# Kernel tuning notes

Measured on AMD Instinct MI355X. Metric: run time of the kernel, lower is better.

## Reference

```python
import jax, jax.numpy as jnp
import numpy as np

B, L, D = 64, 2048, 1024
P, C = 512, 32  # proj_dim = D // 2, score_dim = output_dim
INIT_SCALE = 0.05  # keras 'uniform' init: U(-0.05, 0.05)


def _uniform(key, shape):
    return jax.random.uniform(key, shape, jnp.float32, -INIT_SCALE, INIT_SCALE)


def setup_inputs() -> dict:
    key = jax.random.key(0)
    ks = jax.random.split(key, 8)
    encoded_sentence = jax.random.normal(ks[0], (B, L, D), jnp.float32)
    # indices in [1, L-2] so prep-1 and prep+1 are in bounds
    prep_indices = jax.random.randint(ks[1], (B, 1), 1, L - 1, jnp.int32)
    return {
        "encoded_sentence": encoded_sentence,
        "prep_indices": prep_indices,
        "proj_head": _uniform(ks[2], (D, P)),
        "proj_prep": _uniform(ks[3], (D, P)),
        "proj_child": _uniform(ks[4], (D, P)),
        "hidden_w": _uniform(ks[5], (P, P)),
        "scorer": _uniform(ks[6], (P, C)),
    }


def reference(encoded_sentence, prep_indices, proj_head, proj_prep, proj_child, hidden_w, scorer):
    # encoded_sentence: [B, L, D]; prep_indices: [B, 1]
    prep = prep_indices[:, 0]                      # [B]
    b = jnp.arange(encoded_sentence.shape[0])      # [B]
    head_enc = encoded_sentence[b, prep - 1, :]    # [B, D] (head = token before prep)
    prep_enc = encoded_sentence[b, prep, :]        # [B, D]
    child_enc = encoded_sentence[b, prep + 1, :]   # [B, D]
    # HPCT composition: tanh(sum of three projections)
    composed = jnp.tanh(head_enc @ proj_head + prep_enc @ proj_prep + child_enc @ proj_child)  # [B, P]
    composed = jnp.tanh(composed @ hidden_w)       # one hidden layer
    class_scores = composed @ scorer               # [B, C]
    return jax.nn.softmax(class_scores, axis=-1)
```

## Files before the change

### kernel.cpp

```cpp
#include <hip/hip_runtime.h>
#include <hip/hip_fp16.h>
#include <math.h>

constexpr int B = 64, L = 2048, D = 1024, P = 512, C = 32;
constexpr int CH1 = 64;
constexpr int NK  = 3072 / CH1;
constexpr int G1  = 4 * NK;

constexpr size_t P1_FLOATS = (size_t)NK * B * P;
constexpr size_t OFF_WHIDH = P1_FLOATS;
constexpr size_t OFF_WSCT  = OFF_WHIDH + 131072;

__global__ __launch_bounds__(256) void k1_stage1(
    const float* __restrict__ enc, const int* __restrict__ prep_idx,
    const float* __restrict__ Wh, const float* __restrict__ Wp,
    const float* __restrict__ Wc, const float* __restrict__ Whid,
    const float* __restrict__ Wsc, float* __restrict__ partial1,
    __half* __restrict__ whid_h, __half* __restrict__ wsc_t)
{
    const int tid = threadIdx.x;
    const int ct  = blockIdx.x & 3;
    const int kc  = blockIdx.x >> 2;
    const int m    = kc >> 4;
    const int koff = (kc & 15) * CH1;
    const float* Wm = (m == 0) ? Wh : (m == 1) ? Wp : Wc;

    __shared__ float Xt[CH1][68];
    __shared__ float Wl[CH1][128];

    for (int gid = blockIdx.x * 256 + tid; gid < 65536 + 16384; gid += G1 * 256) {
        if (gid < 65536) {
            const float4 v = *(const float4*)&Whid[(size_t)gid * 4];
            *(__half2*)&whid_h[(size_t)gid * 4]     = __floats2half2_rn(v.x, v.y);
            *(__half2*)&whid_h[(size_t)gid * 4 + 2] = __floats2half2_rn(v.z, v.w);
        } else {
            const int j = gid - 65536;
            const int p = j >> 5, c = j & 31;
            wsc_t[(size_t)c * P + p] = __float2half(Wsc[j]);
        }
    }

    for (int i = tid; i < CH1 * 32; i += 256) {
        const int r = i >> 5, c4 = (i & 31) * 4;
        *(float4*)&Wl[r][c4] =
            *(const float4*)&Wm[(size_t)(koff + r) * P + ct * 128 + c4];
    }
    for (int i = tid; i < 64 * 16; i += 256) {
        const int b = i >> 4, q = i & 15;
        const int row = prep_idx[b] + m - 1;
        const float4 v = *(const float4*)&enc[((size_t)b * L + row) * D + koff + q * 4];
        Xt[q*4+0][b] = v.x; Xt[q*4+1][b] = v.y;
        Xt[q*4+2][b] = v.z; Xt[q*4+3][b] = v.w;
    }
    __syncthreads();

    const int ty = tid >> 4, tx = tid & 15;
    float acc[4][8];
    #pragma unroll
    for (int i = 0; i < 4; ++i)
        #pragma unroll
        for (int j = 0; j < 8; ++j) acc[i][j] = 0.f;

    #pragma unroll 4
    for (int k = 0; k < CH1; ++k) {
        const float4 xv = *(float4*)&Xt[k][ty * 4];
        const float4 w0 = *(float4*)&Wl[k][tx * 8];
        const float4 w1 = *(float4*)&Wl[k][tx * 8 + 4];
        const float xs[4]  = {xv.x, xv.y, xv.z, xv.w};
        const float ws8[8] = {w0.x, w0.y, w0.z, w0.w, w1.x, w1.y, w1.z, w1.w};
        #pragma unroll
        for (int i = 0; i < 4; ++i)
            #pragma unroll
            for (int j = 0; j < 8; ++j) acc[i][j] += xs[i] * ws8[j];
    }

    #pragma unroll
    for (int i = 0; i < 4; ++i) {
        const int b = ty * 4 + i;
        const size_t base = ((size_t)kc * B + b) * P + ct * 128 + tx * 8;
        *(float4*)&partial1[base]     = make_float4(acc[i][0], acc[i][1], acc[i][2], acc[i][3]);
        *(float4*)&partial1[base + 4] = make_float4(acc[i][4], acc[i][5], acc[i][6], acc[i][7]);
    }
}

__global__ __launch_bounds__(512) void k2_tail(
    const float* __restrict__ partial1, const __half* __restrict__ whid_h,
    const __half* __restrict__ wsc_t, float* __restrict__ out)
{
    const int b   = blockIdx.x;
    const int tid = threadIdx.x;

    __shared__ __align__(16) float smem[512 + 4096 + 512 + 16 * 32];
    float* c1s  = smem;
    float* pbuf = smem + 512;
    float* c2s  = smem + 512 + 4096;
    float* sp   = smem + 512 + 4096 + 512;

    {
        const int g = tid >> 7, qq = tid & 127;
        float4 a = make_float4(0.f, 0.f, 0.f, 0.f);
        #pragma unroll 4
        for (int kc = g * 12; kc < g * 12 + 12; ++kc) {
            const float4 v = *(const float4*)&partial1[((size_t)kc * B + b) * P + qq * 4];
            a.x += v.x; a.y += v.y; a.z += v.z; a.w += v.w;
        }
        *(float4*)&pbuf[(g * 128 + qq) * 4] = a;
    }
    __syncthreads();
    {
        const float s = pbuf[tid] + pbuf[512 + tid] + pbuf[1024 + tid] + pbuf[1536 + tid];
        c1s[tid] = tanhf(s);
    }
    __syncthreads();

    {
        const int qo = tid & 63, pg = tid >> 6;
        float a[8];
        #pragma unroll
        for (int j = 0; j < 8; ++j) a[j] = 0.f;
        #pragma unroll 4
        for (int k = 0; k < 64; ++k) {
            const int p = pg * 64 + k;
            const float cv = c1s[p];
            union { uint4 u; __half2 h[4]; } w;
            w.u = *(const uint4*)&whid_h[(size_t)p * P + qo * 8];
            float2 f;
            f = __half22float2(w.h[0]); a[0] += cv * f.x; a[1] += cv * f.y;
            f = __half22float2(w.h[1]); a[2] += cv * f.x; a[3] += cv * f.y;
            f = __half22float2(w.h[2]); a[4] += cv * f.x; a[5] += cv * f.y;
            f = __half22float2(w.h[3]); a[6] += cv * f.x; a[7] += cv * f.y;
        }
        #pragma unroll
        for (int j = 0; j < 8; ++j) pbuf[pg * 512 + qo * 8 + j] = a[j];
    }
    __syncthreads();
    {
        float s = 0.f;
        #pragma unroll
        for (int g = 0; g < 8; ++g) s += pbuf[g * 512 + tid];
        c2s[tid] = tanhf(s);
    }
    __syncthreads();

    {
        const int c = tid & 31, g = tid >> 5;
        float s = 0.f;
        #pragma unroll
        for (int t = 0; t < 4; ++t) {
            const int p0 = g * 32 + t * 8;
            union { uint4 u; __half2 h[4]; } w;
            w.u = *(const uint4*)&wsc_t[(size_t)c * P + p0];
            float2 f;
            f = __half22float2(w.h[0]); s += c2s[p0+0]*f.x + c2s[p0+1]*f.y;
            f = __half22float2(w.h[1]); s += c2s[p0+2]*f.x + c2s[p0+3]*f.y;
            f = __half22float2(w.h[2]); s += c2s[p0+4]*f.x + c2s[p0+5]*f.y;
            f = __half22float2(w.h[3]); s += c2s[p0+6]*f.x + c2s[p0+7]*f.y;
        }
        sp[g * C + c] = s;
    }
    __syncthreads();
    if (tid < C) {
        float sc = 0.f;
        #pragma unroll
        for (int g = 0; g < 16; ++g) sc += sp[g * C + tid];
        float m = sc;
        #pragma unroll
        for (int off = 16; off; off >>= 1) m = fmaxf(m, __shfl_xor(m, off));
        const float e = expf(sc - m);
        float ssum = e;
        #pragma unroll
        for (int off = 16; off; off >>= 1) ssum += __shfl_xor(ssum, off);
        out[b * C + tid] = e / ssum;
    }
}

extern "C" void kernel_launch(void* const* d_in, const int* in_sizes, int n_in,
                              void* d_out, int out_size, void* d_ws, size_t ws_size,
                              hipStream_t stream) {
    const float* enc      = (const float*)d_in[0];
    const int*   prep_idx = (const int*)  d_in[1];
    const float* Wh       = (const float*)d_in[2];
    const float* Wp       = (const float*)d_in[3];
    const float* Wc       = (const float*)d_in[4];
    const float* Whid     = (const float*)d_in[5];
    const float* Wsc      = (const float*)d_in[6];
    float*       out      = (float*)d_out;

    float*  partial1 = (float*)d_ws;
    __half* whid_h   = (__half*)((float*)d_ws + OFF_WHIDH);
    __half* wsc_t    = (__half*)((float*)d_ws + OFF_WSCT);

    (void)in_sizes; (void)n_in; (void)out_size; (void)ws_size;

    k1_stage1<<<G1, 256, 0, stream>>>(enc, prep_idx, Wh, Wp, Wc, Whid, Wsc,
                                      partial1, whid_h, wsc_t);
    k2_tail<<<B, 512, 0, stream>>>(partial1, whid_h, wsc_t, out);
}
```

Before: 24.51 us.

## Store stage-1 partial sums in fp16 and prefetch hidden weights early

Stage one now writes its split-K partial sums as half precision instead of fp32, which halves the intermediate buffer traffic between the two kernels. The tail kernel reduces those halves with 512 threads over 6 chunks each. It also issues the first eight rows of hidden-weight loads before the reduction so their latency overlaps it. Rounding each partial to fp16 before summing adds numerical error, and the prefetch raises register use.

```diff
diff --git a/kernel.cpp b/kernel.cpp
--- a/kernel.cpp
+++ b/kernel.cpp
@@ -7,15 +7,15 @@
 constexpr int NK  = 3072 / CH1;
 constexpr int G1  = 4 * NK;
 
-constexpr size_t P1_FLOATS = (size_t)NK * B * P;
-constexpr size_t OFF_WHIDH = P1_FLOATS;
-constexpr size_t OFF_WSCT  = OFF_WHIDH + 131072;
+constexpr size_t P1_HALFS   = (size_t)NK * B * P;
+constexpr size_t OFF_WHIDH  = P1_HALFS * 2;
+constexpr size_t OFF_WSCT   = OFF_WHIDH + (size_t)P * P * 2;
 
 __global__ __launch_bounds__(256) void k1_stage1(
     const float* __restrict__ enc, const int* __restrict__ prep_idx,
     const float* __restrict__ Wh, const float* __restrict__ Wp,
     const float* __restrict__ Wc, const float* __restrict__ Whid,
-    const float* __restrict__ Wsc, float* __restrict__ partial1,
+    const float* __restrict__ Wsc, __half* __restrict__ partial1h,
     __half* __restrict__ whid_h, __half* __restrict__ wsc_t)
 {
     const int tid = threadIdx.x;
@@ -77,14 +77,16 @@
     #pragma unroll
     for (int i = 0; i < 4; ++i) {
         const int b = ty * 4 + i;
-        const size_t base = ((size_t)kc * B + b) * P + ct * 128 + tx * 8;
-        *(float4*)&partial1[base]     = make_float4(acc[i][0], acc[i][1], acc[i][2], acc[i][3]);
-        *(float4*)&partial1[base + 4] = make_float4(acc[i][4], acc[i][5], acc[i][6], acc[i][7]);
+        union { uint4 u; __half2 h[4]; } pk;
+        #pragma unroll
+        for (int j = 0; j < 4; ++j)
+            pk.h[j] = __floats2half2_rn(acc[i][2*j], acc[i][2*j+1]);
+        *(uint4*)&partial1h[((size_t)kc * B + b) * P + ct * 128 + tx * 8] = pk.u;
     }
 }
 
 __global__ __launch_bounds__(512) void k2_tail(
-    const float* __restrict__ partial1, const __half* __restrict__ whid_h,
+    const __half* __restrict__ partial1h, const __half* __restrict__ whid_h,
     const __half* __restrict__ wsc_t, float* __restrict__ out)
 {
     const int b   = blockIdx.x;
@@ -96,30 +98,56 @@
     float* c2s  = smem + 512 + 4096;
     float* sp   = smem + 512 + 4096 + 512;
 
-    {
-        const int g = tid >> 7, qq = tid & 127;
-        float4 a = make_float4(0.f, 0.f, 0.f, 0.f);
+    const int qo = tid & 63, pg = tid >> 6;
+
+    uint4 pre[8];
+    #pragma unroll
+    for (int k = 0; k < 8; ++k)
+        pre[k] = *(const uint4*)&whid_h[(size_t)(pg * 64 + k) * P + qo * 8];
+
+    {
+        const int g = tid >> 6, p8 = (tid & 63) * 8;
+        float a[8];
+        #pragma unroll
+        for (int j = 0; j < 8; ++j) a[j] = 0.f;
+        #pragma unroll
+        for (int kc = g * 6; kc < g * 6 + 6; ++kc) {
+            union { uint4 u; __half2 h[4]; } w;
+            w.u = *(const uint4*)&partial1h[((size_t)kc * B + b) * P + p8];
+            float2 f;
+            f = __half22float2(w.h[0]); a[0] += f.x; a[1] += f.y;
+            f = __half22float2(w.h[1]); a[2] += f.x; a[3] += f.y;
+            f = __half22float2(w.h[2]); a[4] += f.x; a[5] += f.y;
+            f = __half22float2(w.h[3]); a[6] += f.x; a[7] += f.y;
+        }
+        #pragma unroll
+        for (int j = 0; j < 8; ++j) pbuf[(tid >> 6) * 512 + p8 + j] = a[j];
+    }
+    __syncthreads();
+    {
+        float s = 0.f;
+        #pragma unroll
+        for (int g = 0; g < 8; ++g) s += pbuf[g * 512 + tid];
+        c1s[tid] = tanhf(s);
+    }
+    __syncthreads();
+
+    {
+        float a[8];
+        #pragma unroll
+        for (int j = 0; j < 8; ++j) a[j] = 0.f;
+        #pragma unroll
+        for (int k = 0; k < 8; ++k) {
+            const float cv = c1s[pg * 64 + k];
+            union { uint4 u; __half2 h[4]; } w; w.u = pre[k];
+            float2 f;
+            f = __half22float2(w.h[0]); a[0] += cv * f.x; a[1] += cv * f.y;
+            f = __half22float2(w.h[1]); a[2] += cv * f.x; a[3] += cv * f.y;
+            f = __half22float2(w.h[2]); a[4] += cv * f.x; a[5] += cv * f.y;
+            f = __half22float2(w.h[3]); a[6] += cv * f.x; a[7] += cv * f.y;
+        }
         #pragma unroll 4
-        for (int kc = g * 12; kc < g * 12 + 12; ++kc) {
-            const float4 v = *(const float4*)&partial1[((size_t)kc * B + b) * P + qq * 4];
-            a.x += v.x; a.y += v.y; a.z += v.z; a.w += v.w;
-        }
-        *(float4*)&pbuf[(g * 128 + qq) * 4] = a;
-    }
-    __syncthreads();
-    {
-        const float s = pbuf[tid] + pbuf[512 + tid] + pbuf[1024 + tid] + pbuf[1536 + tid];
-        c1s[tid] = tanhf(s);
-    }
-    __syncthreads();
-
-    {
-        const int qo = tid & 63, pg = tid >> 6;
-        float a[8];
-        #pragma unroll
-        for (int j = 0; j < 8; ++j) a[j] = 0.f;
-        #pragma unroll 4
-        for (int k = 0; k < 64; ++k) {
+        for (int k = 8; k < 64; ++k) {
             const int p = pg * 64 + k;
             const float cv = c1s[p];
             union { uint4 u; __half2 h[4]; } w;
@@ -186,13 +214,13 @@
     const float* Wsc      = (const float*)d_in[6];
     float*       out      = (float*)d_out;
 
-    float*  partial1 = (float*)d_ws;
-    __half* whid_h   = (__half*)((float*)d_ws + OFF_WHIDH);
-    __half* wsc_t    = (__half*)((float*)d_ws + OFF_WSCT);
+    __half* partial1h = (__half*)d_ws;
+    __half* whid_h    = (__half*)((char*)d_ws + OFF_WHIDH);
+    __half* wsc_t     = (__half*)((char*)d_ws + OFF_WSCT);
 
     (void)in_sizes; (void)n_in; (void)out_size; (void)ws_size;
 
     k1_stage1<<<G1, 256, 0, stream>>>(enc, prep_idx, Wh, Wp, Wc, Whid, Wsc,
-                                      partial1, whid_h, wsc_t);
-    k2_tail<<<B, 512, 0, stream>>>(partial1, whid_h, wsc_t, out);
+                                      partial1h, whid_h, wsc_t);
+    k2_tail<<<B, 512, 0, stream>>>(partial1h, whid_h, wsc_t, out);
 }
```

Measured after the change: 23.85 us. 1.03x faster.
